# Kernel tuning notes

Hardware: AMD Instinct MI355X
Metric: run time of the kernel (lower is better)

The kernel has to match this reference:

```python
import jax, jax.numpy as jnp
import numpy as np

B, H, W, C = 8, 32, 32, 256
HEADS, UNITS = 8, 256
OUT_D = UNITS // HEADS          # 32
HID_D = int(OUT_D * 1.0)        # 32 (hidden_rate=1.0)


def setup_inputs() -> dict:
    key = jax.random.key(0)
    ks = jax.random.split(key, 8)
    glorot_qk = np.sqrt(6.0 / (C + HID_D)).astype(np.float32)
    glorot_v = np.sqrt(6.0 / (C + OUT_D)).astype(np.float32)
    return {
        "seq": jax.random.normal(ks[0], (B, H, W, C), dtype=jnp.float32),
        "ctx": jax.random.normal(ks[1], (B, H, W, C), dtype=jnp.float32),
        "Wq": jax.random.uniform(ks[2], (HEADS, C, HID_D), jnp.float32, -glorot_qk, glorot_qk),
        "Wk": jax.random.uniform(ks[3], (HEADS, C, HID_D), jnp.float32, -glorot_qk, glorot_qk),
        "Wv": jax.random.uniform(ks[4], (HEADS, C, OUT_D), jnp.float32, -glorot_v, glorot_v),
        "bq": jnp.zeros((HEADS, HID_D), jnp.float32),
        "bk": jnp.zeros((HEADS, HID_D), jnp.float32),
        "bv": jnp.zeros((HEADS, OUT_D), jnp.float32),
    }


def reference(seq, ctx, Wq, Wk, Wv, bq, bk, bv):
    # NB: the original layer computes q, k, v all from `seq`; `ctx` only fixes
    # the weight shapes. Dropout omitted (inference / deterministic baseline).
    b, h, w, c = seq.shape
    n = h * w
    s = seq.reshape(b, n, c)
    q = jnp.einsum("bnc,hcd->bhnd", s, Wq) + bq[None, :, None, :]
    k = jnp.einsum("bnc,hcd->bhnd", s, Wk) + bk[None, :, None, :]
    v = jnp.einsum("bnc,hcd->bhnd", s, Wv) + bv[None, :, None, :]
    scale = 1.0 / jnp.sqrt(jnp.asarray(k.shape[-1], k.dtype))
    logits = jnp.einsum("bhnd,bhmd->bhnm", q, k * scale)  # [B,heads,N,N]
    attn = jax.nn.softmax(logits, axis=-1)
    a = jnp.einsum("bhnm,bhmd->bhnd", attn, jnp.tanh(v))  # tanh on V, as in source
    out = a.transpose(0, 2, 1, 3).reshape(b, h, w, -1)     # concat heads on channel
    return out
```

## Files before the change

### kernel.cpp

```cpp
#include <hip/hip_runtime.h>
#include <hip/hip_bf16.h>

typedef __attribute__((ext_vector_type(8))) short bf16x8_t;
typedef __attribute__((ext_vector_type(4))) float f32x4_t;
typedef __attribute__((ext_vector_type(16))) float f32x16_t;
typedef __attribute__((ext_vector_type(4))) unsigned short u16x4_t;
typedef __attribute__((ext_vector_type(2))) unsigned u32x2_t;

#define DEVINL __device__ __forceinline__

static constexpr int CN   = 256;
static constexpr int NSEQ = 1024;
static constexpr int NH   = 8;
static constexpr float QSCALE = 0.17677669529663687f * 1.4426950408889634f;

DEVINL unsigned short f2bf(float f) {
    union { __hip_bfloat16 h; unsigned short u; } cv;
    cv.h = __float2bfloat16(f);
    return cv.u;
}

DEVINL unsigned cvtpk_bf16(float lo, float hi) {
    unsigned r;
    asm("v_cvt_pk_bf16_f32 %0, %1, %2" : "=v"(r) : "v"(lo), "v"(hi));
    return r;
}

DEVINL float partner32_f(float x, int h2) {
    unsigned u = __builtin_bit_cast(unsigned, x);
    u32x2_t r = __builtin_amdgcn_permlane32_swap(u, u, false, false);
    return __builtin_bit_cast(float, h2 ? r.x : r.y);
}

DEVINL float fast_tanh(float x) {
    x = fminf(fmaxf(x, -20.f), 20.f);
    float t = __builtin_amdgcn_exp2f(2.8853900817779268f * x);
    return (t - 1.f) * __builtin_amdgcn_rcpf(t + 1.f);
}

__global__ void prep_kernel(const float* __restrict__ Wq, const float* __restrict__ Wk,
                            const float* __restrict__ Wv, const float* __restrict__ seq,
                            unsigned short* __restrict__ Wbt, unsigned short* __restrict__ Sb) {
    if (blockIdx.x < 768) {
        int idx  = blockIdx.x * 256 + threadIdx.x;
        int c    = idx & 255;
        int ncol = idx >> 8;
        int h = ncol / 96, r = ncol % 96;
        int t = r >> 5, d = r & 31;
        const float* W = (t == 0) ? Wq : (t == 1) ? Wk : Wv;
        Wbt[idx] = f2bf(W[((h << 8) + c) * 32 + d]);
    } else {
        int i = (blockIdx.x - 768) * 256 + threadIdx.x;
        const float4 x = ((const float4*)seq)[2 * i];
        const float4 y = ((const float4*)seq)[2 * i + 1];
        union { unsigned u[4]; bf16x8_t v8; } rv;
        rv.u[0] = cvtpk_bf16(x.x, x.y);
        rv.u[1] = cvtpk_bf16(x.z, x.w);
        rv.u[2] = cvtpk_bf16(y.x, y.y);
        rv.u[3] = cvtpk_bf16(y.z, y.w);
        *(bf16x8_t*)(Sb + (size_t)i * 8) = rv.v8;
    }
}

__global__ __launch_bounds__(256) void proj_kernel(
        const unsigned short* __restrict__ Sb, const unsigned short* __restrict__ Wbt,
        const float* __restrict__ bq, const float* __restrict__ bk, const float* __restrict__ bv,
        unsigned short* __restrict__ Qs, unsigned short* __restrict__ Kf,
        unsigned short* __restrict__ Vf) {
    const int w    = threadIdx.x >> 6;
    const int lane = threadIdx.x & 63;
    const int l15  = lane & 15, l4 = lane >> 4;
    const int mw = blockIdx.y * 64 + (w >> 1) * 32;
    const int nw = blockIdx.x * 128 + (w & 1) * 64;

    f32x4_t acc[2][4];
    for (int mg = 0; mg < 2; ++mg)
        for (int g = 0; g < 4; ++g)
            acc[mg][g] = (f32x4_t){0.f, 0.f, 0.f, 0.f};

#pragma unroll
    for (int k0 = 0; k0 < CN; k0 += 32) {
        const int kk = k0 + l4 * 8;
        bf16x8_t a[2], b[4];
        for (int mg = 0; mg < 2; ++mg)
            a[mg] = *(const bf16x8_t*)(Sb + (size_t)(mw + mg * 16 + l15) * CN + kk);
        for (int g = 0; g < 4; ++g)
            b[g] = *(const bf16x8_t*)(Wbt + (size_t)(nw + g * 16 + l15) * CN + kk);
        for (int mg = 0; mg < 2; ++mg)
            for (int g = 0; g < 4; ++g)
                acc[mg][g] = __builtin_amdgcn_mfma_f32_16x16x32_bf16(a[mg], b[g], acc[mg][g], 0, 0, 0);
    }

    for (int g = 0; g < 4; ++g) {
        const int ncol = nw + g * 16;
        const int h = ncol / 96, r = ncol % 96;
        const int t = r >> 5;
        const int d = (r & 31) + l15;
        for (int mg = 0; mg < 2; ++mg) {
            const int m0 = mw + mg * 16 + l4 * 4;
            const int b_ = m0 >> 10;
            const int n0 = m0 & 1023;
            const int bh = b_ * NH + h;
            const int kt = n0 >> 5;
            if (t == 2) {
                const float bias = bv[h * 32 + d];
                u16x4_t vs;
                for (int i = 0; i < 4; ++i)
                    vs[i] = f2bf(fast_tanh(acc[mg][g][i] + bias));
                const size_t fidx = ((size_t)(bh * 32 + kt) * 2 + ((n0 >> 4) & 1)) * 64
                                    + d + 32 * ((n0 >> 3) & 1);
                *(u16x4_t*)(Vf + fidx * 8 + (n0 & 7)) = vs;
            } else if (t == 0) {
                const float bias = bq[h * 32 + d];
                for (int i = 0; i < 4; ++i)
                    Qs[((size_t)bh * NSEQ + n0 + i) * 32 + d] = f2bf((acc[mg][g][i] + bias) * QSCALE);
            } else {
                const float bias = bk[h * 32 + d];
                const size_t fbase = (((size_t)(bh * 32 + kt) * 2 + (d >> 4)) * 64
                                      + 32 * ((d >> 3) & 1)) * 8 + (d & 7);
                for (int i = 0; i < 4; ++i)
                    Kf[fbase + (size_t)((n0 + i) & 31) * 8] = f2bf(acc[mg][g][i] + bias);
            }
        }
    }
}

__global__ __launch_bounds__(256, 4) void attn_kernel(
        const unsigned short* __restrict__ Qs, const unsigned short* __restrict__ Kf,
        const unsigned short* __restrict__ Vf, float* __restrict__ out) {
    __shared__ float comb[2][64][17];
    const int lane = threadIdx.x & 63;
    const int w    = threadIdx.x >> 6;
    const int l31  = lane & 31;
    const int h2   = lane >> 5;
    const int qsel = w >> 1, ksel = w & 1;
    const int id   = blockIdx.x;
    const int slot = id >> 3;
    const int bh   = (id & 7) + 8 * (slot & 7);
    const int qt   = slot >> 3;
    const int b_   = bh >> 3, h = bh & 7;
    const int qrow = qt * 64 + qsel * 32 + l31;

    const unsigned short* Qp = Qs + ((size_t)bh * NSEQ + qrow) * 32 + h2 * 8;
    const bf16x8_t qf0 = *(const bf16x8_t*)(Qp);
    const bf16x8_t qf1 = *(const bf16x8_t*)(Qp + 16);

    const unsigned short* Kp = Kf + (size_t)bh * 32768 + ksel * 16384 + lane * 8;
    const unsigned short* Vp = Vf + (size_t)bh * 32768 + ksel * 16384 + lane * 8;

    f32x16_t o = {0.f,0.f,0.f,0.f,0.f,0.f,0.f,0.f,0.f,0.f,0.f,0.f,0.f,0.f,0.f,0.f};
    float l_acc = 0.f;

    bf16x8_t kf0 = *(const bf16x8_t*)(Kp);
    bf16x8_t kf1 = *(const bf16x8_t*)(Kp + 512);
    bf16x8_t va0 = *(const bf16x8_t*)(Vp);
    bf16x8_t va1 = *(const bf16x8_t*)(Vp + 512);

#pragma unroll
    for (int kt = 0; kt < 16; ++kt) {
        const int ktn = (kt + 1) & 15;
        bf16x8_t nk0 = *(const bf16x8_t*)(Kp + ktn * 1024);
        bf16x8_t nk1 = *(const bf16x8_t*)(Kp + ktn * 1024 + 512);
        bf16x8_t nv0 = *(const bf16x8_t*)(Vp + ktn * 1024);
        bf16x8_t nv1 = *(const bf16x8_t*)(Vp + ktn * 1024 + 512);

        f32x16_t st = {0.f,0.f,0.f,0.f,0.f,0.f,0.f,0.f,0.f,0.f,0.f,0.f,0.f,0.f,0.f,0.f};
        __builtin_amdgcn_s_setprio(1);
        st = __builtin_amdgcn_mfma_f32_32x32x16_bf16(kf0, qf0, st, 0, 0, 0);
        st = __builtin_amdgcn_mfma_f32_32x32x16_bf16(kf1, qf1, st, 0, 0, 0);
        __builtin_amdgcn_s_setprio(0);

        float p[16];
#pragma unroll
        for (int r = 0; r < 16; ++r) p[r] = __builtin_amdgcn_exp2f(st[r]);

        float s8[8];
#pragma unroll
        for (int g = 0; g < 8; ++g) s8[g] = p[2 * g] + p[2 * g + 1];
        float s4a = s8[0] + s8[1], s4b = s8[2] + s8[3];
        float s4c = s8[4] + s8[5], s4d = s8[6] + s8[7];
        l_acc += (s4a + s4b) + (s4c + s4d);

        unsigned pw[8];
#pragma unroll
        for (int g = 0; g < 8; ++g)
            pw[g] = cvtpk_bf16(p[2 * g], p[2 * g + 1]);

        u32x2_t s02 = __builtin_amdgcn_permlane32_swap(pw[0], pw[2], false, false);
        u32x2_t s13 = __builtin_amdgcn_permlane32_swap(pw[1], pw[3], false, false);
        u32x2_t s46 = __builtin_amdgcn_permlane32_swap(pw[4], pw[6], false, false);
        u32x2_t s57 = __builtin_amdgcn_permlane32_swap(pw[5], pw[7], false, false);
        union { unsigned u[4]; bf16x8_t v; } pb1, pb2;
        pb1.u[0] = s02.x; pb1.u[1] = s13.x; pb1.u[2] = s02.y; pb1.u[3] = s13.y;
        pb2.u[0] = s46.x; pb2.u[1] = s57.x; pb2.u[2] = s46.y; pb2.u[3] = s57.y;

        __builtin_amdgcn_s_setprio(1);
        o = __builtin_amdgcn_mfma_f32_32x32x16_bf16(va0, pb1.v, o, 0, 0, 0);
        o = __builtin_amdgcn_mfma_f32_32x32x16_bf16(va1, pb2.v, o, 0, 0, 0);
        __builtin_amdgcn_s_setprio(0);

        kf0 = nk0; kf1 = nk1; va0 = nv0; va1 = nv1;
    }

    const float l_half = l_acc + partner32_f(l_acc, h2);

    if (ksel) {
#pragma unroll
        for (int r = 0; r < 16; ++r) comb[qsel][lane][r] = o[r];
        comb[qsel][lane][16] = l_half;
    }
    __syncthreads();
    if (!ksel) {
        const float* c = comb[qsel][lane];
        const float inv = 1.0f / (l_half + c[16]);
        float* op = out + ((size_t)(b_ * NSEQ + qrow)) * 256 + h * 32 + h2 * 4;
#pragma unroll
        for (int g = 0; g < 4; ++g) {
            float4 q4;
            q4.x = (o[4 * g + 0] + c[4 * g + 0]) * inv;
            q4.y = (o[4 * g + 1] + c[4 * g + 1]) * inv;
            q4.z = (o[4 * g + 2] + c[4 * g + 2]) * inv;
            q4.w = (o[4 * g + 3] + c[4 * g + 3]) * inv;
            *(float4*)(op + 8 * g) = q4;
        }
    }
}

extern "C" void kernel_launch(void* const* d_in, const int* in_sizes, int n_in,
                              void* d_out, int out_size, void* d_ws, size_t ws_size,
                              hipStream_t stream) {
    const float* seq = (const float*)d_in[0];
    const float* Wq = (const float*)d_in[2];
    const float* Wk = (const float*)d_in[3];
    const float* Wv = (const float*)d_in[4];
    const float* bq = (const float*)d_in[5];
    const float* bk = (const float*)d_in[6];
    const float* bv = (const float*)d_in[7];
    float* out = (float*)d_out;

    char* ws = (char*)d_ws;
    unsigned short* Wbt = (unsigned short*)ws;
    unsigned short* Qs  = (unsigned short*)(ws + 393216);
    unsigned short* Kf  = (unsigned short*)(ws + 393216 + 4194304);
    unsigned short* Vf  = (unsigned short*)(ws + 393216 + 2 * 4194304);
    unsigned short* Sb  = (unsigned short*)(ws + 393216 + 3 * 4194304);

    hipLaunchKernelGGL(prep_kernel, dim3(1792), dim3(256), 0, stream, Wq, Wk, Wv, seq, Wbt, Sb);
    hipLaunchKernelGGL(proj_kernel, dim3(6, 128), dim3(256), 0, stream,
                       Sb, Wbt, bq, bk, bv, Qs, Kf, Vf);
    hipLaunchKernelGGL(attn_kernel, dim3(1024), dim3(256), 0, stream, Qs, Kf, Vf, out);
}
```

Measured before the change: 46.41 us.

## Split attention key range four ways per block with 32-row query tiles

Each block now handles 32 query rows, and its four waves each process a quarter of the key sequence (8 tiles instead of 16). Partial outputs and row sums from three waves are combined through shared memory by wave 0. The grid doubles to 2048 blocks and launch bounds target 8 blocks per CU. The goal is more parallelism and a shorter serial loop per wave. In exchange, Q fragments are loaded redundantly and there is more cross-wave reduction traffic.

```diff
diff --git a/kernel.cpp b/kernel.cpp
--- a/kernel.cpp
+++ b/kernel.cpp
@@ -125,28 +125,26 @@
     }
 }
 
-__global__ __launch_bounds__(256, 4) void attn_kernel(
+__global__ __launch_bounds__(256, 8) void attn_kernel(
         const unsigned short* __restrict__ Qs, const unsigned short* __restrict__ Kf,
         const unsigned short* __restrict__ Vf, float* __restrict__ out) {
-    __shared__ float comb[2][64][17];
+    __shared__ float comb[3][64][17];
     const int lane = threadIdx.x & 63;
-    const int w    = threadIdx.x >> 6;
+    const int ksel = threadIdx.x >> 6;
     const int l31  = lane & 31;
     const int h2   = lane >> 5;
-    const int qsel = w >> 1, ksel = w & 1;
-    const int id   = blockIdx.x;
-    const int slot = id >> 3;
-    const int bh   = (id & 7) + 8 * (slot & 7);
-    const int qt   = slot >> 3;
-    const int b_   = bh >> 3, h = bh & 7;
-    const int qrow = qt * 64 + qsel * 32 + l31;
+    const int id = blockIdx.x;
+    const int bh = (id & 7) + 8 * ((id >> 3) & 7);
+    const int qt = id >> 6;
+    const int b_ = bh >> 3, h = bh & 7;
+    const int qrow = qt * 32 + l31;
 
     const unsigned short* Qp = Qs + ((size_t)bh * NSEQ + qrow) * 32 + h2 * 8;
     const bf16x8_t qf0 = *(const bf16x8_t*)(Qp);
     const bf16x8_t qf1 = *(const bf16x8_t*)(Qp + 16);
 
-    const unsigned short* Kp = Kf + (size_t)bh * 32768 + ksel * 16384 + lane * 8;
-    const unsigned short* Vp = Vf + (size_t)bh * 32768 + ksel * 16384 + lane * 8;
+    const unsigned short* Kp = Kf + (size_t)bh * 32768 + ksel * 8192 + lane * 8;
+    const unsigned short* Vp = Vf + (size_t)bh * 32768 + ksel * 8192 + lane * 8;
 
     f32x16_t o = {0.f,0.f,0.f,0.f,0.f,0.f,0.f,0.f,0.f,0.f,0.f,0.f,0.f,0.f,0.f,0.f};
     float l_acc = 0.f;
@@ -157,8 +155,8 @@
     bf16x8_t va1 = *(const bf16x8_t*)(Vp + 512);
 
 #pragma unroll
-    for (int kt = 0; kt < 16; ++kt) {
-        const int ktn = (kt + 1) & 15;
+    for (int kt = 0; kt < 8; ++kt) {
+        const int ktn = (kt + 1) & 7;
         bf16x8_t nk0 = *(const bf16x8_t*)(Kp + ktn * 1024);
         bf16x8_t nk1 = *(const bf16x8_t*)(Kp + ktn * 1024 + 512);
         bf16x8_t nv0 = *(const bf16x8_t*)(Vp + ktn * 1024);
@@ -206,21 +204,23 @@
 
     if (ksel) {
 #pragma unroll
-        for (int r = 0; r < 16; ++r) comb[qsel][lane][r] = o[r];
-        comb[qsel][lane][16] = l_half;
+        for (int r = 0; r < 16; ++r) comb[ksel - 1][lane][r] = o[r];
+        comb[ksel - 1][lane][16] = l_half;
     }
     __syncthreads();
-    if (!ksel) {
-        const float* c = comb[qsel][lane];
-        const float inv = 1.0f / (l_half + c[16]);
+    if (ksel == 0) {
+        const float* c0 = comb[0][lane];
+        const float* c1 = comb[1][lane];
+        const float* c2 = comb[2][lane];
+        const float inv = 1.0f / (l_half + c0[16] + c1[16] + c2[16]);
         float* op = out + ((size_t)(b_ * NSEQ + qrow)) * 256 + h * 32 + h2 * 4;
 #pragma unroll
         for (int g = 0; g < 4; ++g) {
             float4 q4;
-            q4.x = (o[4 * g + 0] + c[4 * g + 0]) * inv;
-            q4.y = (o[4 * g + 1] + c[4 * g + 1]) * inv;
-            q4.z = (o[4 * g + 2] + c[4 * g + 2]) * inv;
-            q4.w = (o[4 * g + 3] + c[4 * g + 3]) * inv;
+            q4.x = (o[4 * g + 0] + c0[4 * g + 0] + c1[4 * g + 0] + c2[4 * g + 0]) * inv;
+            q4.y = (o[4 * g + 1] + c0[4 * g + 1] + c1[4 * g + 1] + c2[4 * g + 1]) * inv;
+            q4.z = (o[4 * g + 2] + c0[4 * g + 2] + c1[4 * g + 2] + c2[4 * g + 2]) * inv;
+            q4.w = (o[4 * g + 3] + c0[4 * g + 3] + c1[4 * g + 3] + c2[4 * g + 3]) * inv;
             *(float4*)(op + 8 * g) = q4;
         }
     }
@@ -248,5 +248,5 @@
     hipLaunchKernelGGL(prep_kernel, dim3(1792), dim3(256), 0, stream, Wq, Wk, Wv, seq, Wbt, Sb);
     hipLaunchKernelGGL(proj_kernel, dim3(6, 128), dim3(256), 0, stream,
                        Sb, Wbt, bq, bk, bv, Qs, Kf, Vf);
-    hipLaunchKernelGGL(attn_kernel, dim3(1024), dim3(256), 0, stream, Qs, Kf, Vf, out);
-}
+    hipLaunchKernelGGL(attn_kernel, dim3(2048), dim3(256), 0, stream, Qs, Kf, Vf, out);
+}
```

After: 95.20 us. 105% more time.

## Process two query tiles per wave to reuse K/V fragments in attention

Applied to the files above, without the earlier changes.

Each wave now computes two 32-row query tiles against the same K/V register fragments, doubling the query rows per block to 128 and halving the grid to 512 blocks. The intent is to halve K/V global loads per query and give each wave two independent MFMA/exp chains to interleave. In exchange register pressure roughly doubles (launch bounds lowered to 2 blocks per SM), and 512 blocks may leave some compute units underused.

```diff
diff --git a/kernel.cpp b/kernel.cpp
--- a/kernel.cpp
+++ b/kernel.cpp
@@ -125,31 +125,34 @@
     }
 }
 
-__global__ __launch_bounds__(256, 4) void attn_kernel(
+__global__ __launch_bounds__(256, 2) void attn_kernel(
         const unsigned short* __restrict__ Qs, const unsigned short* __restrict__ Kf,
         const unsigned short* __restrict__ Vf, float* __restrict__ out) {
-    __shared__ float comb[2][64][17];
+    __shared__ float comb[2][2][64][17];
     const int lane = threadIdx.x & 63;
     const int w    = threadIdx.x >> 6;
     const int l31  = lane & 31;
     const int h2   = lane >> 5;
     const int qsel = w >> 1, ksel = w & 1;
-    const int id   = blockIdx.x;
-    const int slot = id >> 3;
-    const int bh   = (id & 7) + 8 * (slot & 7);
-    const int qt   = slot >> 3;
-    const int b_   = bh >> 3, h = bh & 7;
-    const int qrow = qt * 64 + qsel * 32 + l31;
-
-    const unsigned short* Qp = Qs + ((size_t)bh * NSEQ + qrow) * 32 + h2 * 8;
-    const bf16x8_t qf0 = *(const bf16x8_t*)(Qp);
-    const bf16x8_t qf1 = *(const bf16x8_t*)(Qp + 16);
+    const int id = blockIdx.x;
+    const int bh = (id & 7) + 8 * ((id >> 3) & 7);
+    const int qt = id >> 6;
+    const int b_ = bh >> 3, h = bh & 7;
+    const int qbase = qt * 128 + qsel * 64;
+
+    const unsigned short* Qpa = Qs + ((size_t)bh * NSEQ + qbase + l31) * 32 + h2 * 8;
+    const unsigned short* Qpb = Qpa + 32 * 32;
+    const bf16x8_t qf0a = *(const bf16x8_t*)(Qpa);
+    const bf16x8_t qf1a = *(const bf16x8_t*)(Qpa + 16);
+    const bf16x8_t qf0b = *(const bf16x8_t*)(Qpb);
+    const bf16x8_t qf1b = *(const bf16x8_t*)(Qpb + 16);
 
     const unsigned short* Kp = Kf + (size_t)bh * 32768 + ksel * 16384 + lane * 8;
     const unsigned short* Vp = Vf + (size_t)bh * 32768 + ksel * 16384 + lane * 8;
 
-    f32x16_t o = {0.f,0.f,0.f,0.f,0.f,0.f,0.f,0.f,0.f,0.f,0.f,0.f,0.f,0.f,0.f,0.f};
-    float l_acc = 0.f;
+    f32x16_t oa = {0.f,0.f,0.f,0.f,0.f,0.f,0.f,0.f,0.f,0.f,0.f,0.f,0.f,0.f,0.f,0.f};
+    f32x16_t ob = {0.f,0.f,0.f,0.f,0.f,0.f,0.f,0.f,0.f,0.f,0.f,0.f,0.f,0.f,0.f,0.f};
+    float la = 0.f, lb = 0.f;
 
     bf16x8_t kf0 = *(const bf16x8_t*)(Kp);
     bf16x8_t kf1 = *(const bf16x8_t*)(Kp + 512);
@@ -164,64 +167,107 @@
         bf16x8_t nv0 = *(const bf16x8_t*)(Vp + ktn * 1024);
         bf16x8_t nv1 = *(const bf16x8_t*)(Vp + ktn * 1024 + 512);
 
-        f32x16_t st = {0.f,0.f,0.f,0.f,0.f,0.f,0.f,0.f,0.f,0.f,0.f,0.f,0.f,0.f,0.f,0.f};
-        __builtin_amdgcn_s_setprio(1);
-        st = __builtin_amdgcn_mfma_f32_32x32x16_bf16(kf0, qf0, st, 0, 0, 0);
-        st = __builtin_amdgcn_mfma_f32_32x32x16_bf16(kf1, qf1, st, 0, 0, 0);
-        __builtin_amdgcn_s_setprio(0);
-
-        float p[16];
-#pragma unroll
-        for (int r = 0; r < 16; ++r) p[r] = __builtin_amdgcn_exp2f(st[r]);
-
-        float s8[8];
-#pragma unroll
-        for (int g = 0; g < 8; ++g) s8[g] = p[2 * g] + p[2 * g + 1];
-        float s4a = s8[0] + s8[1], s4b = s8[2] + s8[3];
-        float s4c = s8[4] + s8[5], s4d = s8[6] + s8[7];
-        l_acc += (s4a + s4b) + (s4c + s4d);
-
-        unsigned pw[8];
-#pragma unroll
-        for (int g = 0; g < 8; ++g)
-            pw[g] = cvtpk_bf16(p[2 * g], p[2 * g + 1]);
-
-        u32x2_t s02 = __builtin_amdgcn_permlane32_swap(pw[0], pw[2], false, false);
-        u32x2_t s13 = __builtin_amdgcn_permlane32_swap(pw[1], pw[3], false, false);
-        u32x2_t s46 = __builtin_amdgcn_permlane32_swap(pw[4], pw[6], false, false);
-        u32x2_t s57 = __builtin_amdgcn_permlane32_swap(pw[5], pw[7], false, false);
-        union { unsigned u[4]; bf16x8_t v; } pb1, pb2;
-        pb1.u[0] = s02.x; pb1.u[1] = s13.x; pb1.u[2] = s02.y; pb1.u[3] = s13.y;
-        pb2.u[0] = s46.x; pb2.u[1] = s57.x; pb2.u[2] = s46.y; pb2.u[3] = s57.y;
-
-        __builtin_amdgcn_s_setprio(1);
-        o = __builtin_amdgcn_mfma_f32_32x32x16_bf16(va0, pb1.v, o, 0, 0, 0);
-        o = __builtin_amdgcn_mfma_f32_32x32x16_bf16(va1, pb2.v, o, 0, 0, 0);
-        __builtin_amdgcn_s_setprio(0);
+        {
+            f32x16_t st = {0.f,0.f,0.f,0.f,0.f,0.f,0.f,0.f,0.f,0.f,0.f,0.f,0.f,0.f,0.f,0.f};
+            __builtin_amdgcn_s_setprio(1);
+            st = __builtin_amdgcn_mfma_f32_32x32x16_bf16(kf0, qf0a, st, 0, 0, 0);
+            st = __builtin_amdgcn_mfma_f32_32x32x16_bf16(kf1, qf1a, st, 0, 0, 0);
+            __builtin_amdgcn_s_setprio(0);
+            float p[16];
+#pragma unroll
+            for (int r = 0; r < 16; ++r) p[r] = __builtin_amdgcn_exp2f(st[r]);
+            float s8[8];
+#pragma unroll
+            for (int g = 0; g < 8; ++g) s8[g] = p[2 * g] + p[2 * g + 1];
+            la += ((s8[0] + s8[1]) + (s8[2] + s8[3])) + ((s8[4] + s8[5]) + (s8[6] + s8[7]));
+            unsigned pw[8];
+#pragma unroll
+            for (int g = 0; g < 8; ++g) pw[g] = cvtpk_bf16(p[2 * g], p[2 * g + 1]);
+            u32x2_t s02 = __builtin_amdgcn_permlane32_swap(pw[0], pw[2], false, false);
+            u32x2_t s13 = __builtin_amdgcn_permlane32_swap(pw[1], pw[3], false, false);
+            u32x2_t s46 = __builtin_amdgcn_permlane32_swap(pw[4], pw[6], false, false);
+            u32x2_t s57 = __builtin_amdgcn_permlane32_swap(pw[5], pw[7], false, false);
+            union { unsigned u[4]; bf16x8_t v; } pb1, pb2;
+            pb1.u[0] = s02.x; pb1.u[1] = s13.x; pb1.u[2] = s02.y; pb1.u[3] = s13.y;
+            pb2.u[0] = s46.x; pb2.u[1] = s57.x; pb2.u[2] = s46.y; pb2.u[3] = s57.y;
+            __builtin_amdgcn_s_setprio(1);
+            oa = __builtin_amdgcn_mfma_f32_32x32x16_bf16(va0, pb1.v, oa, 0, 0, 0);
+            oa = __builtin_amdgcn_mfma_f32_32x32x16_bf16(va1, pb2.v, oa, 0, 0, 0);
+            __builtin_amdgcn_s_setprio(0);
+        }
+        {
+            f32x16_t st = {0.f,0.f,0.f,0.f,0.f,0.f,0.f,0.f,0.f,0.f,0.f,0.f,0.f,0.f,0.f,0.f};
+            __builtin_amdgcn_s_setprio(1);
+            st = __builtin_amdgcn_mfma_f32_32x32x16_bf16(kf0, qf0b, st, 0, 0, 0);
+            st = __builtin_amdgcn_mfma_f32_32x32x16_bf16(kf1, qf1b, st, 0, 0, 0);
+            __builtin_amdgcn_s_setprio(0);
+            float p[16];
+#pragma unroll
+            for (int r = 0; r < 16; ++r) p[r] = __builtin_amdgcn_exp2f(st[r]);
+            float s8[8];
+#pragma unroll
+            for (int g = 0; g < 8; ++g) s8[g] = p[2 * g] + p[2 * g + 1];
+            lb += ((s8[0] + s8[1]) + (s8[2] + s8[3])) + ((s8[4] + s8[5]) + (s8[6] + s8[7]));
+            unsigned pw[8];
+#pragma unroll
+            for (int g = 0; g < 8; ++g) pw[g] = cvtpk_bf16(p[2 * g], p[2 * g + 1]);
+            u32x2_t s02 = __builtin_amdgcn_permlane32_swap(pw[0], pw[2], false, false);
+            u32x2_t s13 = __builtin_amdgcn_permlane32_swap(pw[1], pw[3], false, false);
+            u32x2_t s46 = __builtin_amdgcn_permlane32_swap(pw[4], pw[6], false, false);
+            u32x2_t s57 = __builtin_amdgcn_permlane32_swap(pw[5], pw[7], false, false);
+            union { unsigned u[4]; bf16x8_t v; } pb1, pb2;
+            pb1.u[0] = s02.x; pb1.u[1] = s13.x; pb1.u[2] = s02.y; pb1.u[3] = s13.y;
+            pb2.u[0] = s46.x; pb2.u[1] = s57.x; pb2.u[2] = s46.y; pb2.u[3] = s57.y;
+            __builtin_amdgcn_s_setprio(1);
+            ob = __builtin_amdgcn_mfma_f32_32x32x16_bf16(va0, pb1.v, ob, 0, 0, 0);
+            ob = __builtin_amdgcn_mfma_f32_32x32x16_bf16(va1, pb2.v, ob, 0, 0, 0);
+            __builtin_amdgcn_s_setprio(0);
+        }
 
         kf0 = nk0; kf1 = nk1; va0 = nv0; va1 = nv1;
     }
 
-    const float l_half = l_acc + partner32_f(l_acc, h2);
+    const float lha = la + partner32_f(la, h2);
+    const float lhb = lb + partner32_f(lb, h2);
 
     if (ksel) {
 #pragma unroll
-        for (int r = 0; r < 16; ++r) comb[qsel][lane][r] = o[r];
-        comb[qsel][lane][16] = l_half;
+        for (int r = 0; r < 16; ++r) {
+            comb[qsel][0][lane][r] = oa[r];
+            comb[qsel][1][lane][r] = ob[r];
+        }
+        comb[qsel][0][lane][16] = lha;
+        comb[qsel][1][lane][16] = lhb;
     }
     __syncthreads();
     if (!ksel) {
-        const float* c = comb[qsel][lane];
-        const float inv = 1.0f / (l_half + c[16]);
-        float* op = out + ((size_t)(b_ * NSEQ + qrow)) * 256 + h * 32 + h2 * 4;
-#pragma unroll
-        for (int g = 0; g < 4; ++g) {
-            float4 q4;
-            q4.x = (o[4 * g + 0] + c[4 * g + 0]) * inv;
-            q4.y = (o[4 * g + 1] + c[4 * g + 1]) * inv;
-            q4.z = (o[4 * g + 2] + c[4 * g + 2]) * inv;
-            q4.w = (o[4 * g + 3] + c[4 * g + 3]) * inv;
-            *(float4*)(op + 8 * g) = q4;
+        {
+            const float* c = comb[qsel][0][lane];
+            const float inv = 1.0f / (lha + c[16]);
+            float* op = out + ((size_t)(b_ * NSEQ + qbase + l31)) * 256 + h * 32 + h2 * 4;
+#pragma unroll
+            for (int g = 0; g < 4; ++g) {
+                float4 q4;
+                q4.x = (oa[4 * g + 0] + c[4 * g + 0]) * inv;
+                q4.y = (oa[4 * g + 1] + c[4 * g + 1]) * inv;
+                q4.z = (oa[4 * g + 2] + c[4 * g + 2]) * inv;
+                q4.w = (oa[4 * g + 3] + c[4 * g + 3]) * inv;
+                *(float4*)(op + 8 * g) = q4;
+            }
+        }
+        {
+            const float* c = comb[qsel][1][lane];
+            const float inv = 1.0f / (lhb + c[16]);
+            float* op = out + ((size_t)(b_ * NSEQ + qbase + 32 + l31)) * 256 + h * 32 + h2 * 4;
+#pragma unroll
+            for (int g = 0; g < 4; ++g) {
+                float4 q4;
+                q4.x = (ob[4 * g + 0] + c[4 * g + 0]) * inv;
+                q4.y = (ob[4 * g + 1] + c[4 * g + 1]) * inv;
+                q4.z = (ob[4 * g + 2] + c[4 * g + 2]) * inv;
+                q4.w = (ob[4 * g + 3] + c[4 * g + 3]) * inv;
+                *(float4*)(op + 8 * g) = q4;
+            }
         }
     }
 }
@@ -248,5 +294,5 @@
     hipLaunchKernelGGL(prep_kernel, dim3(1792), dim3(256), 0, stream, Wq, Wk, Wv, seq, Wbt, Sb);
     hipLaunchKernelGGL(proj_kernel, dim3(6, 128), dim3(256), 0, stream,
                        Sb, Wbt, bq, bk, bv, Qs, Kf, Vf);
-    hipLaunchKernelGGL(attn_kernel, dim3(1024), dim3(256), 0, stream, Qs, Kf, Vf, out);
-}
+    hipLaunchKernelGGL(attn_kernel, dim3(512), dim3(256), 0, stream, Qs, Kf, Vf, out);
+}
```

New measurement: 45.83 us, median of 2. About the same (-1.2%).

## Process four Q subtiles per wave to reuse K/V fragments across more queries

Applied to the files above, without the earlier changes.

Each attention block now handles 256 query rows instead of 64, with each wave holding four 32-row Q fragments and looping over them for every K/V tile. K and V fragments loaded from global memory are reused four times, cutting K/V traffic and load instructions per query. The grid drops from 1024 to 256 blocks (about one per CU on MI355X), and launch bounds are relaxed to one block per SM, so register use per thread grows. Occupancy and latency hiding drop in exchange.

```diff
diff --git a/kernel.cpp b/kernel.cpp
--- a/kernel.cpp
+++ b/kernel.cpp
@@ -125,31 +125,39 @@
     }
 }
 
-__global__ __launch_bounds__(256, 4) void attn_kernel(
+__global__ __launch_bounds__(256, 1) void attn_kernel(
         const unsigned short* __restrict__ Qs, const unsigned short* __restrict__ Kf,
         const unsigned short* __restrict__ Vf, float* __restrict__ out) {
-    __shared__ float comb[2][64][17];
+    __shared__ float comb[2][4][64][17];
     const int lane = threadIdx.x & 63;
     const int w    = threadIdx.x >> 6;
     const int l31  = lane & 31;
     const int h2   = lane >> 5;
     const int qsel = w >> 1, ksel = w & 1;
-    const int id   = blockIdx.x;
-    const int slot = id >> 3;
-    const int bh   = (id & 7) + 8 * (slot & 7);
-    const int qt   = slot >> 3;
-    const int b_   = bh >> 3, h = bh & 7;
-    const int qrow = qt * 64 + qsel * 32 + l31;
-
-    const unsigned short* Qp = Qs + ((size_t)bh * NSEQ + qrow) * 32 + h2 * 8;
-    const bf16x8_t qf0 = *(const bf16x8_t*)(Qp);
-    const bf16x8_t qf1 = *(const bf16x8_t*)(Qp + 16);
+    const int id = blockIdx.x;
+    const int bh = (id & 7) + 8 * ((id >> 3) & 7);
+    const int qt = id >> 6;
+    const int b_ = bh >> 3, h = bh & 7;
+    const int qbase = qt * 256 + qsel * 128;
+
+    bf16x8_t qf0[4], qf1[4];
+#pragma unroll
+    for (int s = 0; s < 4; ++s) {
+        const unsigned short* Qp = Qs + ((size_t)bh * NSEQ + qbase + s * 32 + l31) * 32 + h2 * 8;
+        qf0[s] = *(const bf16x8_t*)(Qp);
+        qf1[s] = *(const bf16x8_t*)(Qp + 16);
+    }
 
     const unsigned short* Kp = Kf + (size_t)bh * 32768 + ksel * 16384 + lane * 8;
     const unsigned short* Vp = Vf + (size_t)bh * 32768 + ksel * 16384 + lane * 8;
 
-    f32x16_t o = {0.f,0.f,0.f,0.f,0.f,0.f,0.f,0.f,0.f,0.f,0.f,0.f,0.f,0.f,0.f,0.f};
-    float l_acc = 0.f;
+    f32x16_t o[4];
+    float lac[4];
+#pragma unroll
+    for (int s = 0; s < 4; ++s) {
+        o[s] = (f32x16_t){0.f,0.f,0.f,0.f,0.f,0.f,0.f,0.f,0.f,0.f,0.f,0.f,0.f,0.f,0.f,0.f};
+        lac[s] = 0.f;
+    }
 
     bf16x8_t kf0 = *(const bf16x8_t*)(Kp);
     bf16x8_t kf1 = *(const bf16x8_t*)(Kp + 512);
@@ -164,64 +172,70 @@
         bf16x8_t nv0 = *(const bf16x8_t*)(Vp + ktn * 1024);
         bf16x8_t nv1 = *(const bf16x8_t*)(Vp + ktn * 1024 + 512);
 
-        f32x16_t st = {0.f,0.f,0.f,0.f,0.f,0.f,0.f,0.f,0.f,0.f,0.f,0.f,0.f,0.f,0.f,0.f};
-        __builtin_amdgcn_s_setprio(1);
-        st = __builtin_amdgcn_mfma_f32_32x32x16_bf16(kf0, qf0, st, 0, 0, 0);
-        st = __builtin_amdgcn_mfma_f32_32x32x16_bf16(kf1, qf1, st, 0, 0, 0);
-        __builtin_amdgcn_s_setprio(0);
-
-        float p[16];
-#pragma unroll
-        for (int r = 0; r < 16; ++r) p[r] = __builtin_amdgcn_exp2f(st[r]);
-
-        float s8[8];
-#pragma unroll
-        for (int g = 0; g < 8; ++g) s8[g] = p[2 * g] + p[2 * g + 1];
-        float s4a = s8[0] + s8[1], s4b = s8[2] + s8[3];
-        float s4c = s8[4] + s8[5], s4d = s8[6] + s8[7];
-        l_acc += (s4a + s4b) + (s4c + s4d);
-
-        unsigned pw[8];
-#pragma unroll
-        for (int g = 0; g < 8; ++g)
-            pw[g] = cvtpk_bf16(p[2 * g], p[2 * g + 1]);
-
-        u32x2_t s02 = __builtin_amdgcn_permlane32_swap(pw[0], pw[2], false, false);
-        u32x2_t s13 = __builtin_amdgcn_permlane32_swap(pw[1], pw[3], false, false);
-        u32x2_t s46 = __builtin_amdgcn_permlane32_swap(pw[4], pw[6], false, false);
-        u32x2_t s57 = __builtin_amdgcn_permlane32_swap(pw[5], pw[7], false, false);
-        union { unsigned u[4]; bf16x8_t v; } pb1, pb2;
-        pb1.u[0] = s02.x; pb1.u[1] = s13.x; pb1.u[2] = s02.y; pb1.u[3] = s13.y;
-        pb2.u[0] = s46.x; pb2.u[1] = s57.x; pb2.u[2] = s46.y; pb2.u[3] = s57.y;
-
-        __builtin_amdgcn_s_setprio(1);
-        o = __builtin_amdgcn_mfma_f32_32x32x16_bf16(va0, pb1.v, o, 0, 0, 0);
-        o = __builtin_amdgcn_mfma_f32_32x32x16_bf16(va1, pb2.v, o, 0, 0, 0);
-        __builtin_amdgcn_s_setprio(0);
+#pragma unroll
+        for (int s = 0; s < 4; ++s) {
+            f32x16_t st = {0.f,0.f,0.f,0.f,0.f,0.f,0.f,0.f,0.f,0.f,0.f,0.f,0.f,0.f,0.f,0.f};
+            __builtin_amdgcn_s_setprio(1);
+            st = __builtin_amdgcn_mfma_f32_32x32x16_bf16(kf0, qf0[s], st, 0, 0, 0);
+            st = __builtin_amdgcn_mfma_f32_32x32x16_bf16(kf1, qf1[s], st, 0, 0, 0);
+            __builtin_amdgcn_s_setprio(0);
+
+            float p[16];
+#pragma unroll
+            for (int r = 0; r < 16; ++r) p[r] = __builtin_amdgcn_exp2f(st[r]);
+            float s8[8];
+#pragma unroll
+            for (int g = 0; g < 8; ++g) s8[g] = p[2 * g] + p[2 * g + 1];
+            lac[s] += ((s8[0] + s8[1]) + (s8[2] + s8[3])) + ((s8[4] + s8[5]) + (s8[6] + s8[7]));
+
+            unsigned pw[8];
+#pragma unroll
+            for (int g = 0; g < 8; ++g) pw[g] = cvtpk_bf16(p[2 * g], p[2 * g + 1]);
+            u32x2_t s02 = __builtin_amdgcn_permlane32_swap(pw[0], pw[2], false, false);
+            u32x2_t s13 = __builtin_amdgcn_permlane32_swap(pw[1], pw[3], false, false);
+            u32x2_t s46 = __builtin_amdgcn_permlane32_swap(pw[4], pw[6], false, false);
+            u32x2_t s57 = __builtin_amdgcn_permlane32_swap(pw[5], pw[7], false, false);
+            union { unsigned u[4]; bf16x8_t v; } pb1, pb2;
+            pb1.u[0] = s02.x; pb1.u[1] = s13.x; pb1.u[2] = s02.y; pb1.u[3] = s13.y;
+            pb2.u[0] = s46.x; pb2.u[1] = s57.x; pb2.u[2] = s46.y; pb2.u[3] = s57.y;
+
+            __builtin_amdgcn_s_setprio(1);
+            o[s] = __builtin_amdgcn_mfma_f32_32x32x16_bf16(va0, pb1.v, o[s], 0, 0, 0);
+            o[s] = __builtin_amdgcn_mfma_f32_32x32x16_bf16(va1, pb2.v, o[s], 0, 0, 0);
+            __builtin_amdgcn_s_setprio(0);
+        }
 
         kf0 = nk0; kf1 = nk1; va0 = nv0; va1 = nv1;
     }
 
-    const float l_half = l_acc + partner32_f(l_acc, h2);
+    float lh[4];
+#pragma unroll
+    for (int s = 0; s < 4; ++s) lh[s] = lac[s] + partner32_f(lac[s], h2);
 
     if (ksel) {
 #pragma unroll
-        for (int r = 0; r < 16; ++r) comb[qsel][lane][r] = o[r];
-        comb[qsel][lane][16] = l_half;
+        for (int s = 0; s < 4; ++s) {
+#pragma unroll
+            for (int r = 0; r < 16; ++r) comb[qsel][s][lane][r] = o[s][r];
+            comb[qsel][s][lane][16] = lh[s];
+        }
     }
     __syncthreads();
     if (!ksel) {
-        const float* c = comb[qsel][lane];
-        const float inv = 1.0f / (l_half + c[16]);
-        float* op = out + ((size_t)(b_ * NSEQ + qrow)) * 256 + h * 32 + h2 * 4;
-#pragma unroll
-        for (int g = 0; g < 4; ++g) {
-            float4 q4;
-            q4.x = (o[4 * g + 0] + c[4 * g + 0]) * inv;
-            q4.y = (o[4 * g + 1] + c[4 * g + 1]) * inv;
-            q4.z = (o[4 * g + 2] + c[4 * g + 2]) * inv;
-            q4.w = (o[4 * g + 3] + c[4 * g + 3]) * inv;
-            *(float4*)(op + 8 * g) = q4;
+#pragma unroll
+        for (int s = 0; s < 4; ++s) {
+            const float* c = comb[qsel][s][lane];
+            const float inv = 1.0f / (lh[s] + c[16]);
+            float* op = out + ((size_t)(b_ * NSEQ + qbase + s * 32 + l31)) * 256 + h * 32 + h2 * 4;
+#pragma unroll
+            for (int g = 0; g < 4; ++g) {
+                float4 q4;
+                q4.x = (o[s][4 * g + 0] + c[4 * g + 0]) * inv;
+                q4.y = (o[s][4 * g + 1] + c[4 * g + 1]) * inv;
+                q4.z = (o[s][4 * g + 2] + c[4 * g + 2]) * inv;
+                q4.w = (o[s][4 * g + 3] + c[4 * g + 3]) * inv;
+                *(float4*)(op + 8 * g) = q4;
+            }
         }
     }
 }
@@ -248,5 +262,5 @@
     hipLaunchKernelGGL(prep_kernel, dim3(1792), dim3(256), 0, stream, Wq, Wk, Wv, seq, Wbt, Sb);
     hipLaunchKernelGGL(proj_kernel, dim3(6, 128), dim3(256), 0, stream,
                        Sb, Wbt, bq, bk, bv, Qs, Kf, Vf);
-    hipLaunchKernelGGL(attn_kernel, dim3(1024), dim3(256), 0, stream, Qs, Kf, Vf, out);
-}
+    hipLaunchKernelGGL(attn_kernel, dim3(256), dim3(256), 0, stream, Qs, Kf, Vf, out);
+}
```

Result: slower. 50.42 us (+8.6%).
